# Kernel optimization log

Measured on AMD Instinct MI355X. Metric: run time of the kernel, lower is better.

Reference implementation:

```python
import jax, jax.numpy as jnp
import numpy as np
import math

B, S, D = 2, 1024, 2048
NH, NKV, HD = 16, 8, 128
NREP = NH // NKV
WINDOW = 256  # = max_seq_len; ReRoPE window


def _rope(x, cos, sin):
    # x: (b, s, h, d); cos/sin broadcastable to (b, s, h, d//2). Interleaved pairs (llama2.c style).
    b, s, h, d = x.shape
    xr, xi = x[..., ::2], x[..., 1::2]
    or_ = xr * cos - xi * sin
    oi = xr * sin + xi * cos
    return jnp.stack([or_, oi], axis=-1).reshape(b, s, h, d)


def setup_inputs() -> dict:
    key = jax.random.key(0)
    kx, kq, kk, kv, ko = jax.random.split(key, 5)
    # real RoPE tables (theta=10000), per-position, half head dim
    inv = 1.0 / (10000.0 ** (np.arange(0, HD, 2, dtype=np.float32) / HD))
    fr = np.outer(np.arange(S, dtype=np.float32), inv).astype(np.float32)  # (S, HD//2)
    sc = 0.02
    return {
        "x": jax.random.normal(kx, (B, S, D), jnp.float32),
        "freqs_cos": jnp.asarray(np.cos(fr)),
        "freqs_sin": jnp.asarray(np.sin(fr)),
        "wq": jax.random.normal(kq, (D, NH * HD), jnp.float32) * sc,
        "wk": jax.random.normal(kk, (D, NKV * HD), jnp.float32) * sc,
        "wv": jax.random.normal(kv, (D, NKV * HD), jnp.float32) * sc,
        "wo": jax.random.normal(ko, (NH * HD, D), jnp.float32) * sc,
    }


def reference(x, freqs_cos, freqs_sin, wq, wk, wv, wo):
    b, s, _ = x.shape
    xq = (x @ wq).reshape(b, s, NH, HD)
    xk = (x @ wk).reshape(b, s, NKV, HD)
    xv = (x @ wv).reshape(b, s, NKV, HD)

    cos = freqs_cos[:s][None, :, None, :]
    sin = freqs_sin[:s][None, :, None, :]
    q1 = _rope(xq, cos, sin)   # standard RoPE
    k1 = _rope(xk, cos, sin)

    # ReRoPE: queries rotated at the fixed clamp position = window; keys unrotated
    cw = freqs_cos[WINDOW][None, None, None, :]
    sw = freqs_sin[WINDOW][None, None, None, :]
    q2 = _rope(xq, cw, sw)
    k2 = xk

    rep = lambda a: jnp.repeat(a, NREP, axis=2)          # repeat_kv (GQA)
    heads = lambda a: a.transpose(0, 2, 1, 3)            # (b, h, s, d)
    q1, k1, v = heads(q1), heads(rep(k1)), heads(rep(xv))
    q2, k2 = heads(q2), heads(rep(k2))

    scale = 1.0 / math.sqrt(HD)
    s1 = jnp.einsum("bhqd,bhkd->bhqk", q1, k1) * scale
    s2 = jnp.einsum("bhqd,bhkd->bhqk", q2, k2) * scale

    i = jnp.arange(s)[:, None]
    j = jnp.arange(s)[None, :]
    causal = j <= i
    rect = causal & (j > i - WINDOW)                     # rectified_mask band
    scores = jnp.where(rect, s1, s2)
    scores = jnp.where(causal, scores, -jnp.inf)         # mask_inf (causal)

    attn = jax.nn.softmax(scores.astype(jnp.float32), axis=-1).astype(x.dtype)
    out = jnp.einsum("bhqk,bhkd->bhqd", attn, v)
    out = out.transpose(0, 2, 1, 3).reshape(b, s, NH * HD)
    return out @ wo
```

## Files before the change

kernel.cpp:

```cpp
#include <hip/hip_runtime.h>
#include <hip/hip_bf16.h>

#define BDIM 2
#define SDIM 1024
#define DDIM 2048
#define NH 16
#define NKV 8
#define HD 128
#define WINDOW 256

typedef __bf16 bf16;
typedef __bf16 bf16x4 __attribute__((ext_vector_type(4)));
typedef __bf16 bf16x8 __attribute__((ext_vector_type(8)));
typedef float f32x4 __attribute__((ext_vector_type(4)));

#define L2E 1.44269504088896341f

__device__ inline bf16x8 load8(const bf16* p) { return *reinterpret_cast<const bf16x8*>(p); }

__device__ __forceinline__ void gl_lds16(const bf16* g, bf16* l) {
  __builtin_amdgcn_global_load_lds(
      (__attribute__((address_space(1))) void*)g,
      (__attribute__((address_space(3))) void*)l,
      16, 0, 0);
}

__global__ __launch_bounds__(256) void prep(const float* __restrict__ x,
                                            const float* __restrict__ wq,
                                            const float* __restrict__ wk,
                                            const float* __restrict__ wv,
                                            const float* __restrict__ wo,
                                            bf16* __restrict__ xb,
                                            bf16* __restrict__ wqkvT,
                                            bf16* __restrict__ woT) {
  __shared__ bf16 tile[32][33];
  int z = blockIdx.z;
  int tx = threadIdx.x, ty = threadIdx.y;
  if (z == 4) {
    long i = (((long)blockIdx.y * 64 + blockIdx.x) * 256 + ty * 32 + tx) * 4;
    float4 a = *(const float4*)(x + i);
    bf16x4 o;
    o[0] = (bf16)a.x; o[1] = (bf16)a.y; o[2] = (bf16)a.z; o[3] = (bf16)a.w;
    *(bf16x4*)(xb + i) = o;
    return;
  }
  const float* src; bf16* dst; int C;
  if (z == 0)      { src = wq; dst = wqkvT;                 C = 2048; }
  else if (z == 1) { src = wk; dst = wqkvT + 2048L * 2048;  C = 1024; }
  else if (z == 2) { src = wv; dst = wqkvT + 3072L * 2048;  C = 1024; }
  else             { src = wo; dst = woT;                   C = 2048; }
  int c0 = blockIdx.x * 32, r0 = blockIdx.y * 32;
  if (c0 >= C) return;
  for (int yy = ty; yy < 32; yy += 8)
    tile[yy][tx] = (bf16)src[(long)(r0 + yy) * C + c0 + tx];
  __syncthreads();
  for (int yy = ty; yy < 32; yy += 8)
    dst[(long)(c0 + yy) * 2048 + r0 + tx] = tile[tx][yy];
}

#define BK 64
__global__ __launch_bounds__(256) void gemm_bt_n64(const bf16* __restrict__ A,
                                                   const bf16* __restrict__ Bt,
                                                   float* __restrict__ C,
                                                   int M, int N, int K) {
  __shared__ bf16 As[128 * BK];
  __shared__ bf16 Bs[64 * BK];
  int m0 = blockIdx.y * 128, n0 = blockIdx.x * 64;
  int t = threadIdx.x;
  int wid = t >> 6, lane = t & 63;
  int wm = (wid >> 1) * 64, wn = (wid & 1) * 32;
  int fm = lane & 15, quad = lane >> 4;
  f32x4 acc[4][2] = {};
  for (int k0 = 0; k0 < K; k0 += BK) {
    for (int p = 0; p < 4; ++p) {
      int idx = p * 256 + t;
      int row = idx >> 3, ccs = idx & 7;
      int gcol = ((ccs ^ (row & 7)) * 8);
      gl_lds16(&A[(long)(m0 + row) * K + k0 + gcol], &As[idx * 8]);
    }
    for (int p = 0; p < 2; ++p) {
      int idx = p * 256 + t;
      int row = idx >> 3, ccs = idx & 7;
      int gcol = ((ccs ^ (row & 7)) * 8);
      gl_lds16(&Bt[(long)(n0 + row) * K + k0 + gcol], &Bs[idx * 8]);
    }
    __syncthreads();
    for (int ks = 0; ks < BK; ks += 32) {
      int cc = (ks >> 3) + quad;
      bf16x8 af[4], bfr[2];
      for (int i = 0; i < 4; ++i) {
        int fr = wm + i * 16 + fm;
        af[i] = load8(&As[(fr * 8 + (cc ^ (fr & 7))) * 8]);
      }
      for (int j = 0; j < 2; ++j) {
        int fr = wn + j * 16 + fm;
        bfr[j] = load8(&Bs[(fr * 8 + (cc ^ (fr & 7))) * 8]);
      }
      for (int i = 0; i < 4; ++i)
        for (int j = 0; j < 2; ++j)
          acc[i][j] = __builtin_amdgcn_mfma_f32_16x16x32_bf16(af[i], bfr[j], acc[i][j], 0, 0, 0);
    }
    __syncthreads();
  }
  for (int i = 0; i < 4; ++i)
    for (int r = 0; r < 4; ++r) {
      int row = m0 + wm + i * 16 + quad * 4 + r;
      for (int j = 0; j < 2; ++j) {
        int col = n0 + wn + j * 16 + fm;
        C[(long)row * N + col] = acc[i][j][r];
      }
    }
}

#define VPITCH 130
__global__ __launch_bounds__(256) void gemm_qkv(const bf16* __restrict__ A,
                                                const bf16* __restrict__ Bt,
                                                const float* __restrict__ fc,
                                                const float* __restrict__ fs,
                                                bf16* __restrict__ q0,
                                                bf16* __restrict__ k1,
                                                bf16* __restrict__ k2,
                                                bf16* __restrict__ vT) {
  const int K = 2048;
  __shared__ bf16 smem[128 * VPITCH];
  bf16* As = smem;
  bf16* Bs = smem + 8192;
  int m0 = blockIdx.y * 128, n0 = blockIdx.x * 128;
  int t = threadIdx.x;
  int wid = t >> 6, lane = t & 63;
  int wm = (wid >> 1) * 64, wn = (wid & 1) * 64;
  int fm = lane & 15, quad = lane >> 4;
  f32x4 acc[4][4] = {};
  for (int k0 = 0; k0 < K; k0 += BK) {
    for (int p = 0; p < 4; ++p) {
      int idx = p * 256 + t;
      int row = idx >> 3, ccs = idx & 7;
      int gcol = ((ccs ^ (row & 7)) * 8);
      gl_lds16(&A[(long)(m0 + row) * K + k0 + gcol], &As[idx * 8]);
      gl_lds16(&Bt[(long)(n0 + row) * K + k0 + gcol], &Bs[idx * 8]);
    }
    __syncthreads();
    for (int ks = 0; ks < BK; ks += 32) {
      int cc = (ks >> 3) + quad;
      bf16x8 af[4], bfr[4];
      for (int i = 0; i < 4; ++i) {
        int fr = wm + i * 16 + fm;
        af[i] = load8(&As[(fr * 8 + (cc ^ (fr & 7))) * 8]);
      }
      for (int i = 0; i < 4; ++i) {
        int fr = wn + i * 16 + fm;
        bfr[i] = load8(&Bs[(fr * 8 + (cc ^ (fr & 7))) * 8]);
      }
      for (int i = 0; i < 4; ++i)
        for (int j = 0; j < 4; ++j)
          acc[i][j] = __builtin_amdgcn_mfma_f32_16x16x32_bf16(af[i], bfr[j], acc[i][j], 0, 0, 0);
    }
    __syncthreads();
  }

  int n0h = n0 >> 7;
  if (n0h < 16) {
    const float scale = 0.08838834764831845f;
    for (int i = 0; i < 4; ++i)
      for (int r = 0; r < 4; ++r) {
        int row = m0 + wm + i * 16 + quad * 4 + r;
        for (int j = 0; j < 4; ++j) {
          int col = wn + j * 16 + fm;
          q0[(long)row * 2048 + n0h * 128 + col] = (bf16)(acc[i][j][r] * scale);
        }
      }
  } else if (n0h < 24) {
    int kvh = n0h - 16;
    float sgn = (lane & 1) ? 1.f : -1.f;
    float cwj[4], swj[4];
    for (int j = 0; j < 4; ++j) {
      int dp = (wn + j * 16 + fm) >> 1;
      cwj[j] = fc[WINDOW * 64 + dp];
      swj[j] = fs[WINDOW * 64 + dp] * (-sgn);
    }
    for (int i = 0; i < 4; ++i)
      for (int r = 0; r < 4; ++r) {
        int row = m0 + wm + i * 16 + quad * 4 + r;
        int s = row & (SDIM - 1);
        for (int j = 0; j < 4; ++j) {
          int col = wn + j * 16 + fm;
          int dp = col >> 1;
          float v = acc[i][j][r];
          float pp = __shfl_xor(v, 1, 64);
          float c = fc[s * 64 + dp];
          float sn = fs[s * 64 + dp] * sgn;
          long dst = (long)row * 1024 + kvh * 128 + col;
          k1[dst] = (bf16)(v * c + pp * sn);
          k2[dst] = (bf16)(v * cwj[j] + pp * swj[j]);
        }
      }
  } else {
    int vv = n0h - 24;
    for (int i = 0; i < 4; ++i)
      for (int j = 0; j < 4; ++j) {
        int col = wn + j * 16 + fm;
        for (int r = 0; r < 4; ++r) {
          int rl = wm + i * 16 + quad * 4 + r;
          smem[col * VPITCH + rl] = (bf16)acc[i][j][r];
        }
      }
    __syncthreads();
    int s0l = m0 & (SDIM - 1);
    int bq = m0 >> 10;
    bf16* vtg = vT + ((long)(bq * NKV + vv)) * 128 * 1024;
    for (int p = 0; p < 8; ++p) {
      int c = p * 256 + t;
      int d = c >> 4, sc = (c & 15) * 8;
      *(bf16x8*)&vtg[(long)d * 1024 + s0l + sc] = *(bf16x8*)&smem[d * VPITCH + sc];
    }
  }
}

__global__ __launch_bounds__(256) void attn_kernel(const bf16* __restrict__ q0,
                                                   const bf16* __restrict__ k1,
                                                   const bf16* __restrict__ k2,
                                                   const bf16* __restrict__ vT,
                                                   const float* __restrict__ fc,
                                                   const float* __restrict__ fs,
                                                   bf16* __restrict__ aout) {
  __shared__ bf16 Ks[16384];
  __shared__ bf16 VTs[8192];
  __shared__ bf16 Pl[4][16][72];
  __shared__ float stats[4][16];

  int h = blockIdx.y;
  int b = blockIdx.z;
  int tile = b ? (15 - blockIdx.x) : blockIdx.x;
  int kv = h >> 1;
  int t = threadIdx.x;
  int w = t >> 6, lane = t & 63;
  int m = lane & 15, quad = lane >> 4;

  const bf16* k1g0 = k1 + ((long)b * SDIM) * 1024 + kv * 128;
  const bf16* k2g0 = k2 + ((long)b * SDIM) * 1024 + kv * 128;
  const bf16* vtg0 = vT + ((long)(b * NKV + kv)) * 128 * 1024;

  int t0 = tile * 64;
  int i0w = t0 + w * 16;

  const bf16* q0p = q0 + ((long)(b * SDIM + i0w + m)) * 2048 + h * 128 + quad * 8;
  bf16x8 q0f[4], q1f[4];
  int srow = i0w + m;
  for (int kc = 0; kc < 4; ++kc) {
    q0f[kc] = load8(q0p + kc * 32);
    for (int p4 = 0; p4 < 4; ++p4) {
      int dp = kc * 16 + quad * 4 + p4;
      float c = fc[srow * 64 + dp], sn = fs[srow * 64 + dp];
      float xr = (float)q0f[kc][2 * p4], xi = (float)q0f[kc][2 * p4 + 1];
      q1f[kc][2 * p4]     = (bf16)(xr * c - xi * sn);
      q1f[kc][2 * p4 + 1] = (bf16)(xr * sn + xi * c);
    }
  }

  f32x4 o[8] = {};
  float mrow = -INFINITY, lrow = 0.f;

  for (int j0 = 0; j0 < t0 + 64; j0 += 64) {
    bool c1 = (j0 + 63 > t0 - WINDOW);
    bool c2 = (j0 <= t0 + 63 - WINDOW);
    __syncthreads();
    for (int p = 0; p < 4; ++p) {
      int idx = p * 256 + t;
      int kr = idx >> 4, kcs = idx & 15;
      int kg = (kcs ^ (kr & 15)) * 8;
      if (c1) gl_lds16(&k1g0[(long)(j0 + kr) * 1024 + kg], &Ks[idx * 8]);
      if (c2) gl_lds16(&k2g0[(long)(j0 + kr) * 1024 + kg], &Ks[8192 + idx * 8]);
      int vd = idx >> 3, vcs = idx & 7;
      int vg = (vcs ^ (vd & 7)) * 8;
      gl_lds16(&vtg0[(long)vd * 1024 + j0 + vg], &VTs[idx * 8]);
    }
    __syncthreads();

    if (j0 < i0w + 16) {
      bool need1 = (j0 + 63 > i0w - WINDOW);
      bool need2 = (j0 <= i0w + 15 - WINDOW);
      f32x4 s1[4] = {}, s2[4] = {};
      if (need1)
        for (int st = 0; st < 4; ++st)
          for (int kc = 0; kc < 4; ++kc) {
            int cc = kc * 4 + quad;
            s1[st] = __builtin_amdgcn_mfma_f32_16x16x32_bf16(
                load8(&Ks[((st * 16 + m) * 16 + (cc ^ m)) * 8]), q1f[kc], s1[st], 0, 0, 0);
          }
      if (need2)
        for (int st = 0; st < 4; ++st)
          for (int kc = 0; kc < 4; ++kc) {
            int cc = kc * 4 + quad;
            s2[st] = __builtin_amdgcn_mfma_f32_16x16x32_bf16(
                load8(&Ks[8192 + ((st * 16 + m) * 16 + (cc ^ m)) * 8]), q0f[kc], s2[st], 0, 0, 0);
          }
      int i = i0w + m;
      float sv[4][4];
      for (int st = 0; st < 4; ++st)
        for (int r = 0; r < 4; ++r) {
          int j = j0 + st * 16 + quad * 4 + r;
          float v;
          if (j > i) v = -INFINITY;
          else if (j > i - WINDOW) v = s1[st][r];
          else v = s2[st][r];
          sv[st][r] = v;
        }
      float bm = -INFINITY;
      for (int st = 0; st < 4; ++st)
        for (int r = 0; r < 4; ++r) bm = fmaxf(bm, sv[st][r]);
      bm = fmaxf(bm, __shfl_xor(bm, 16, 64));
      bm = fmaxf(bm, __shfl_xor(bm, 32, 64));
      float mnew = fmaxf(mrow, bm);
      float alpha = exp2f((mrow - mnew) * L2E);
      float rs = 0.f;
      for (int st = 0; st < 4; ++st) {
        bf16x4 pk;
        for (int r = 0; r < 4; ++r) {
          float pvv = exp2f((sv[st][r] - mnew) * L2E);
          rs += pvv;
          pk[r] = (bf16)pvv;
        }
        *(bf16x4*)&Pl[w][m][st * 16 + quad * 4] = pk;
      }
      rs += __shfl_xor(rs, 16, 64);
      rs += __shfl_xor(rs, 32, 64);
      lrow = lrow * alpha + rs;
      mrow = mnew;
      if (lane < 16) stats[w][lane] = alpha;
      f32x4 av = *(f32x4*)&stats[w][quad * 4];
      for (int n8 = 0; n8 < 8; ++n8)
        for (int r = 0; r < 4; ++r) o[n8][r] *= av[r];
      for (int kc = 0; kc < 2; ++kc) {
        bf16x8 af = load8(&Pl[w][m][kc * 32 + quad * 8]);
        int cc = kc * 4 + quad;
        for (int n8 = 0; n8 < 8; ++n8) {
          int d = n8 * 16 + m;
          o[n8] = __builtin_amdgcn_mfma_f32_16x16x32_bf16(
              af, load8(&VTs[(d * 8 + (cc ^ (d & 7))) * 8]), o[n8], 0, 0, 0);
        }
      }
    }
  }

  if (lane < 16) stats[w][lane] = lrow;
  __builtin_amdgcn_s_waitcnt(0);
  f32x4 lv = *(f32x4*)&stats[w][quad * 4];
  for (int n8 = 0; n8 < 8; ++n8)
    for (int r = 0; r < 4; ++r) {
      int row = i0w + quad * 4 + r;
      float val = o[n8][r] / lv[r];
      aout[((long)(b * SDIM + row)) * 2048 + h * 128 + n8 * 16 + m] = (bf16)val;
    }
}

extern "C" void kernel_launch(void* const* d_in, const int* in_sizes, int n_in,
                              void* d_out, int out_size, void* d_ws, size_t ws_size,
                              hipStream_t stream) {
  const float* x  = (const float*)d_in[0];
  const float* fc = (const float*)d_in[1];
  const float* fs = (const float*)d_in[2];
  const float* wq = (const float*)d_in[3];
  const float* wk = (const float*)d_in[4];
  const float* wv = (const float*)d_in[5];
  const float* wo = (const float*)d_in[6];
  float* out = (float*)d_out;

  bf16* wqkvT = (bf16*)d_ws;
  bf16* woT   = wqkvT + 4096L * 2048;
  bf16* xb    = woT + 2048L * 2048;
  bf16* q0b   = xb + 2048L * 2048;
  bf16* k1b   = q0b + 2048L * 2048;
  bf16* k2b   = k1b + 2048L * 1024;
  bf16* vT    = k2b + 2048L * 1024;
  bf16* aout  = vT + 2048L * 1024;

  prep<<<dim3(64, 64, 5), dim3(32, 8), 0, stream>>>(x, wq, wk, wv, wo, xb, wqkvT, woT);

  gemm_qkv<<<dim3(32, 16), 256, 0, stream>>>(xb, wqkvT, fc, fs, q0b, k1b, k2b, vT);

  attn_kernel<<<dim3(16, 16, 2), 256, 0, stream>>>(q0b, k1b, k2b, vT, fc, fs, aout);

  gemm_bt_n64<<<dim3(32, 16), 256, 0, stream>>>(aout, woT, out, 2048, 2048, 2048);
}
```

Before: 240.4 us.

## Double-buffer LDS in both GEMMs, swizzle block order, widen QKV tile

Both projection GEMMs now double-buffer their LDS tiles. The next K-slice loads via global_load_lds are issued while MFMAs run on the current slice, using manual vmcnt waits and barriers. The workgroup index is remapped so neighbouring blocks share operand rows in L2, and MFMA sections raise wave priority. The QKV GEMM moves to 512-thread blocks with a 128x256 tile and writes the V transpose in two halves. The aim is to hide global load latency and improve cache reuse, at the cost of more LDS per block and possibly lower occupancy.

Result: faster. 226.0 us (-6.0%).

```diff
diff --git a/kernel.cpp b/kernel.cpp
--- a/kernel.cpp
+++ b/kernel.cpp
@@ -63,44 +63,77 @@
                                                    const bf16* __restrict__ Bt,
                                                    float* __restrict__ C,
                                                    int M, int N, int K) {
-  __shared__ bf16 As[128 * BK];
-  __shared__ bf16 Bs[64 * BK];
-  int m0 = blockIdx.y * 128, n0 = blockIdx.x * 64;
+  __shared__ bf16 smem[2 * 12288];
   int t = threadIdx.x;
   int wid = t >> 6, lane = t & 63;
   int wm = (wid >> 1) * 64, wn = (wid & 1) * 32;
   int fm = lane & 15, quad = lane >> 4;
+
+  int wg = blockIdx.y * 32 + blockIdx.x;
+  int swz = (wg & 7) * 64 + (wg >> 3);
+  int by = swz >> 5, bx = swz & 31;
+  int m0 = by * 128, n0 = bx * 64;
+
+  const bf16* Ag = A + (long)m0 * K;
+  const bf16* Bg = Bt + (long)n0 * K;
+
   f32x4 acc[4][2] = {};
-  for (int k0 = 0; k0 < K; k0 += BK) {
-    for (int p = 0; p < 4; ++p) {
-      int idx = p * 256 + t;
-      int row = idx >> 3, ccs = idx & 7;
-      int gcol = ((ccs ^ (row & 7)) * 8);
-      gl_lds16(&A[(long)(m0 + row) * K + k0 + gcol], &As[idx * 8]);
-    }
-    for (int p = 0; p < 2; ++p) {
-      int idx = p * 256 + t;
-      int row = idx >> 3, ccs = idx & 7;
-      int gcol = ((ccs ^ (row & 7)) * 8);
-      gl_lds16(&Bt[(long)(n0 + row) * K + k0 + gcol], &Bs[idx * 8]);
-    }
-    __syncthreads();
-    for (int ks = 0; ks < BK; ks += 32) {
-      int cc = (ks >> 3) + quad;
-      bf16x8 af[4], bfr[2];
-      for (int i = 0; i < 4; ++i) {
-        int fr = wm + i * 16 + fm;
-        af[i] = load8(&As[(fr * 8 + (cc ^ (fr & 7))) * 8]);
-      }
-      for (int j = 0; j < 2; ++j) {
-        int fr = wn + j * 16 + fm;
-        bfr[j] = load8(&Bs[(fr * 8 + (cc ^ (fr & 7))) * 8]);
-      }
-      for (int i = 0; i < 4; ++i)
-        for (int j = 0; j < 2; ++j)
-          acc[i][j] = __builtin_amdgcn_mfma_f32_16x16x32_bf16(af[i], bfr[j], acc[i][j], 0, 0, 0);
-    }
-    __syncthreads();
+
+  auto stA = [&](bf16* dst, int k0, int p) {
+    int idx = p * 256 + t;
+    int row = idx >> 3, ccs = idx & 7;
+    int gcol = ((ccs ^ (row & 7)) * 8);
+    gl_lds16(&Ag[(long)row * K + k0 + gcol], &dst[idx * 8]);
+  };
+  auto stB = [&](bf16* dst, int k0, int p) {
+    int idx = p * 256 + t;
+    int row = idx >> 3, ccs = idx & 7;
+    int gcol = ((ccs ^ (row & 7)) * 8);
+    gl_lds16(&Bg[(long)row * K + k0 + gcol], &dst[idx * 8]);
+  };
+  auto cmp = [&](const bf16* As, const bf16* Bs, int ks) {
+    int cc = (ks >> 3) + quad;
+    bf16x8 af[4], bfr[2];
+    for (int i = 0; i < 4; ++i) {
+      int fr = wm + i * 16 + fm;
+      af[i] = load8(&As[(fr * 8 + (cc ^ (fr & 7))) * 8]);
+    }
+    for (int j = 0; j < 2; ++j) {
+      int fr = wn + j * 16 + fm;
+      bfr[j] = load8(&Bs[(fr * 8 + (cc ^ (fr & 7))) * 8]);
+    }
+    __builtin_amdgcn_s_setprio(1);
+    for (int i = 0; i < 4; ++i)
+      for (int j = 0; j < 2; ++j)
+        acc[i][j] = __builtin_amdgcn_mfma_f32_16x16x32_bf16(af[i], bfr[j], acc[i][j], 0, 0, 0);
+    __builtin_amdgcn_s_setprio(0);
+  };
+
+  {
+    bf16* As = smem; bf16* Bs = smem + 8192;
+    stA(As, 0, 0); stA(As, 0, 1); stA(As, 0, 2); stA(As, 0, 3);
+    stB(Bs, 0, 0); stB(Bs, 0, 1);
+  }
+  const int NT = K / BK;
+  for (int kt = 0; kt < NT; ++kt) {
+    int cur = kt & 1;
+    bf16* As = smem + cur * 12288;
+    bf16* Bs = As + 8192;
+    if (kt + 1 < NT) {
+      bf16* An = smem + (cur ^ 1) * 12288;
+      bf16* Bn = An + 8192;
+      int kn = (kt + 1) * BK;
+      stA(An, kn, 0); stA(An, kn, 1); stB(Bn, kn, 0);
+      asm volatile("s_waitcnt vmcnt(3)\n\ts_barrier" ::: "memory");
+      cmp(As, Bs, 0);
+      stA(An, kn, 2); stA(An, kn, 3); stB(Bn, kn, 1);
+      cmp(As, Bs, 32);
+      asm volatile("s_barrier" ::: "memory");
+    } else {
+      asm volatile("s_waitcnt vmcnt(0)\n\ts_barrier" ::: "memory");
+      cmp(As, Bs, 0);
+      cmp(As, Bs, 32);
+    }
   }
   for (int i = 0; i < 4; ++i)
     for (int r = 0; r < 4; ++r) {
@@ -113,7 +146,7 @@
 }
 
 #define VPITCH 130
-__global__ __launch_bounds__(256) void gemm_qkv(const bf16* __restrict__ A,
+__global__ __launch_bounds__(512) void gemm_qkv(const bf16* __restrict__ A,
                                                 const bf16* __restrict__ Bt,
                                                 const float* __restrict__ fc,
                                                 const float* __restrict__ fs,
@@ -122,59 +155,94 @@
                                                 bf16* __restrict__ k2,
                                                 bf16* __restrict__ vT) {
   const int K = 2048;
-  __shared__ bf16 smem[128 * VPITCH];
-  bf16* As = smem;
-  bf16* Bs = smem + 8192;
-  int m0 = blockIdx.y * 128, n0 = blockIdx.x * 128;
+  __shared__ bf16 smem[2 * 24576];
   int t = threadIdx.x;
   int wid = t >> 6, lane = t & 63;
-  int wm = (wid >> 1) * 64, wn = (wid & 1) * 64;
+  int wm = (wid >> 2) * 64, wn = (wid & 3) * 64;
   int fm = lane & 15, quad = lane >> 4;
+
+  int wg = blockIdx.y * 16 + blockIdx.x;
+  int swz = (wg & 7) * 32 + (wg >> 3);
+  int by = swz >> 4, bx = swz & 15;
+  int m0 = by * 128, n0 = bx * 256;
+
+  const bf16* Ag = A + (long)m0 * K;
+  const bf16* Bg = Bt + (long)n0 * K;
+
   f32x4 acc[4][4] = {};
-  for (int k0 = 0; k0 < K; k0 += BK) {
-    for (int p = 0; p < 4; ++p) {
-      int idx = p * 256 + t;
-      int row = idx >> 3, ccs = idx & 7;
-      int gcol = ((ccs ^ (row & 7)) * 8);
-      gl_lds16(&A[(long)(m0 + row) * K + k0 + gcol], &As[idx * 8]);
-      gl_lds16(&Bt[(long)(n0 + row) * K + k0 + gcol], &Bs[idx * 8]);
-    }
-    __syncthreads();
-    for (int ks = 0; ks < BK; ks += 32) {
-      int cc = (ks >> 3) + quad;
-      bf16x8 af[4], bfr[4];
-      for (int i = 0; i < 4; ++i) {
-        int fr = wm + i * 16 + fm;
-        af[i] = load8(&As[(fr * 8 + (cc ^ (fr & 7))) * 8]);
-      }
-      for (int i = 0; i < 4; ++i) {
-        int fr = wn + i * 16 + fm;
-        bfr[i] = load8(&Bs[(fr * 8 + (cc ^ (fr & 7))) * 8]);
-      }
-      for (int i = 0; i < 4; ++i)
-        for (int j = 0; j < 4; ++j)
-          acc[i][j] = __builtin_amdgcn_mfma_f32_16x16x32_bf16(af[i], bfr[j], acc[i][j], 0, 0, 0);
-    }
-    __syncthreads();
-  }
-
-  int n0h = n0 >> 7;
-  if (n0h < 16) {
+
+  auto stA = [&](bf16* dst, int k0, int p) {
+    int idx = p * 512 + t;
+    int row = idx >> 3, ccs = idx & 7;
+    int gcol = ((ccs ^ (row & 7)) * 8);
+    gl_lds16(&Ag[(long)row * K + k0 + gcol], &dst[idx * 8]);
+  };
+  auto stB = [&](bf16* dst, int k0, int p) {
+    int idx = p * 512 + t;
+    int row = idx >> 3, ccs = idx & 7;
+    int gcol = ((ccs ^ (row & 7)) * 8);
+    gl_lds16(&Bg[(long)row * K + k0 + gcol], &dst[idx * 8]);
+  };
+  auto cmp = [&](const bf16* As, const bf16* Bs, int ks) {
+    int cc = (ks >> 3) + quad;
+    bf16x8 af[4], bfr[4];
+    for (int i = 0; i < 4; ++i) {
+      int fr = wm + i * 16 + fm;
+      af[i] = load8(&As[(fr * 8 + (cc ^ (fr & 7))) * 8]);
+    }
+    for (int j = 0; j < 4; ++j) {
+      int fr = wn + j * 16 + fm;
+      bfr[j] = load8(&Bs[(fr * 8 + (cc ^ (fr & 7))) * 8]);
+    }
+    __builtin_amdgcn_s_setprio(1);
+    for (int i = 0; i < 4; ++i)
+      for (int j = 0; j < 4; ++j)
+        acc[i][j] = __builtin_amdgcn_mfma_f32_16x16x32_bf16(af[i], bfr[j], acc[i][j], 0, 0, 0);
+    __builtin_amdgcn_s_setprio(0);
+  };
+
+  {
+    bf16* As = smem; bf16* Bs = smem + 8192;
+    stA(As, 0, 0); stA(As, 0, 1);
+    stB(Bs, 0, 0); stB(Bs, 0, 1); stB(Bs, 0, 2); stB(Bs, 0, 3);
+  }
+  const int NT = K / 64;
+  for (int kt = 0; kt < NT; ++kt) {
+    int cur = kt & 1;
+    bf16* As = smem + cur * 24576;
+    bf16* Bs = As + 8192;
+    if (kt + 1 < NT) {
+      bf16* An = smem + (cur ^ 1) * 24576;
+      bf16* Bn = An + 8192;
+      int kn = (kt + 1) * 64;
+      stA(An, kn, 0); stA(An, kn, 1); stB(Bn, kn, 0);
+      asm volatile("s_waitcnt vmcnt(3)\n\ts_barrier" ::: "memory");
+      cmp(As, Bs, 0);
+      stB(Bn, kn, 1); stB(Bn, kn, 2); stB(Bn, kn, 3);
+      cmp(As, Bs, 32);
+      asm volatile("s_barrier" ::: "memory");
+    } else {
+      asm volatile("s_waitcnt vmcnt(0)\n\ts_barrier" ::: "memory");
+      cmp(As, Bs, 0);
+      cmp(As, Bs, 32);
+    }
+  }
+
+  if (n0 < 2048) {
     const float scale = 0.08838834764831845f;
     for (int i = 0; i < 4; ++i)
       for (int r = 0; r < 4; ++r) {
         int row = m0 + wm + i * 16 + quad * 4 + r;
         for (int j = 0; j < 4; ++j) {
-          int col = wn + j * 16 + fm;
-          q0[(long)row * 2048 + n0h * 128 + col] = (bf16)(acc[i][j][r] * scale);
+          int gc = n0 + wn + j * 16 + fm;
+          q0[(long)row * 2048 + gc] = (bf16)(acc[i][j][r] * scale);
         }
       }
-  } else if (n0h < 24) {
-    int kvh = n0h - 16;
+  } else if (n0 < 3072) {
     float sgn = (lane & 1) ? 1.f : -1.f;
     float cwj[4], swj[4];
     for (int j = 0; j < 4; ++j) {
-      int dp = (wn + j * 16 + fm) >> 1;
+      int dp = ((wn + j * 16 + fm) & 127) >> 1;
       cwj[j] = fc[WINDOW * 64 + dp];
       swj[j] = fs[WINDOW * 64 + dp] * (-sgn);
     }
@@ -183,35 +251,40 @@
         int row = m0 + wm + i * 16 + quad * 4 + r;
         int s = row & (SDIM - 1);
         for (int j = 0; j < 4; ++j) {
-          int col = wn + j * 16 + fm;
-          int dp = col >> 1;
+          int kc = n0 - 2048 + wn + j * 16 + fm;
+          int dp = (kc & 127) >> 1;
           float v = acc[i][j][r];
           float pp = __shfl_xor(v, 1, 64);
           float c = fc[s * 64 + dp];
           float sn = fs[s * 64 + dp] * sgn;
-          long dst = (long)row * 1024 + kvh * 128 + col;
+          long dst = (long)row * 1024 + kc;
           k1[dst] = (bf16)(v * c + pp * sn);
           k2[dst] = (bf16)(v * cwj[j] + pp * swj[j]);
         }
       }
   } else {
-    int vv = n0h - 24;
-    for (int i = 0; i < 4; ++i)
-      for (int j = 0; j < 4; ++j) {
-        int col = wn + j * 16 + fm;
-        for (int r = 0; r < 4; ++r) {
-          int rl = wm + i * 16 + quad * 4 + r;
-          smem[col * VPITCH + rl] = (bf16)acc[i][j][r];
-        }
-      }
-    __syncthreads();
+    int vv0 = (n0 - 3072) >> 7;
     int s0l = m0 & (SDIM - 1);
     int bq = m0 >> 10;
-    bf16* vtg = vT + ((long)(bq * NKV + vv)) * 128 * 1024;
-    for (int p = 0; p < 8; ++p) {
-      int c = p * 256 + t;
-      int d = c >> 4, sc = (c & 15) * 8;
-      *(bf16x8*)&vtg[(long)d * 1024 + s0l + sc] = *(bf16x8*)&smem[d * VPITCH + sc];
+    for (int half = 0; half < 2; ++half) {
+      __syncthreads();
+      if (((wn >> 7) & 1) == half) {
+        for (int i = 0; i < 4; ++i)
+          for (int j = 0; j < 4; ++j) {
+            int col = (wn & 127) + j * 16 + fm;
+            for (int r = 0; r < 4; ++r) {
+              int rl = wm + i * 16 + quad * 4 + r;
+              smem[col * VPITCH + rl] = (bf16)acc[i][j][r];
+            }
+          }
+      }
+      __syncthreads();
+      bf16* vtg = vT + ((long)(bq * NKV + vv0 + half)) * 128 * 1024;
+      for (int p = 0; p < 4; ++p) {
+        int c = p * 512 + t;
+        int d = c >> 4, sc = (c & 15) * 8;
+        *(bf16x8*)&vtg[(long)d * 1024 + s0l + sc] = *(bf16x8*)&smem[d * VPITCH + sc];
+      }
     }
   }
 }
@@ -376,7 +449,7 @@
 
   prep<<<dim3(64, 64, 5), dim3(32, 8), 0, stream>>>(x, wq, wk, wv, wo, xb, wqkvT, woT);
 
-  gemm_qkv<<<dim3(32, 16), 256, 0, stream>>>(xb, wqkvT, fc, fs, q0b, k1b, k2b, vT);
+  gemm_qkv<<<dim3(16, 16), 512, 0, stream>>>(xb, wqkvT, fc, fs, q0b, k1b, k2b, vT);
 
   attn_kernel<<<dim3(16, 16, 2), 256, 0, stream>>>(q0b, k1b, k2b, vT, fc, fs, aout);
 
```
